# Optimization experiments

Hardware: AMD Instinct MI355X
Metric: run time of the kernel (lower is better)

## Reference

```python
import jax, jax.numpy as jnp
import numpy as np

H = 128          # input hidden dim
HID = 128        # expert hidden width
OUT = 128        # out_channels
NR = 8           # n_routed
NS = 2           # n_shared
RDIM = 16        # router feature dim


def setup_inputs() -> dict:
    key = jax.random.key(0)
    ks = jax.random.split(key, 11)
    s = 0.05
    x = jax.random.normal(ks[0], (2, 32, 32, 32, H), dtype=jnp.float32)
    # router params
    Wr1 = jax.random.normal(ks[1], (H, RDIM), dtype=jnp.float32) * s
    br1 = jnp.zeros((RDIM,), dtype=jnp.float32)
    Wr2 = jax.random.normal(ks[2], (RDIM, NR), dtype=jnp.float32) * s
    br2 = jnp.zeros((NR,), dtype=jnp.float32)
    # routed expert params, stacked on leading expert axis
    We1 = jax.random.normal(ks[3], (NR, H, HID), dtype=jnp.float32) * s
    be1 = jnp.zeros((NR, HID), dtype=jnp.float32)
    We2 = jax.random.normal(ks[4], (NR, HID, OUT), dtype=jnp.float32) * s
    be2 = jnp.zeros((NR, OUT), dtype=jnp.float32)
    # shared expert params
    Ws1 = jax.random.normal(ks[5], (NS, H, HID), dtype=jnp.float32) * s
    bs1 = jnp.zeros((NS, HID), dtype=jnp.float32)
    Ws2 = jax.random.normal(ks[6], (NS, HID, OUT), dtype=jnp.float32) * s
    bs2 = jnp.zeros((NS, OUT), dtype=jnp.float32)
    return dict(x=x, Wr1=Wr1, br1=br1, Wr2=Wr2, br2=br2,
                We1=We1, be1=be1, We2=We2, be2=be2,
                Ws1=Ws1, bs1=bs1, Ws2=Ws2, bs2=bs2)


def reference(x, Wr1, br1, Wr2, br2, We1, be1, We2, be2, Ws1, bs1, Ws2, bs2):
    # router: Dense(16) -> relu -> Dense(n_routed) -> softmax
    rf = jax.nn.relu(jnp.einsum('...h,hr->...r', x, Wr1) + br1)
    logits = jnp.einsum('...r,re->...e', rf, Wr2) + br2
    gate = jax.nn.softmax(logits, axis=-1)                      # [..., NR]
    threshold = 1.0 / NR
    mask = (gate > threshold).astype(gate.dtype)
    mg = gate * mask
    mg = mg / (jnp.sum(mg, axis=-1, keepdims=True) + 1e-8)
    # routed experts (batched over expert axis e): Dense -> gelu(tanh) -> Dense
    hr = jax.nn.gelu(jnp.einsum('...h,ehd->...ed', x, We1) + be1)   # [..., NR, HID]
    ro = jnp.einsum('...ed,edo->...eo', hr, We2) + be2              # [..., NR, OUT]
    routed_agg = jnp.einsum('...eo,...e->...o', ro, mg)
    # shared experts summed
    hs = jax.nn.gelu(jnp.einsum('...h,ehd->...ed', x, Ws1) + bs1)   # [..., NS, HID]
    so = jnp.einsum('...ed,edo->...eo', hs, Ws2) + bs2              # [..., NS, OUT]
    shared_agg = jnp.sum(so, axis=-2)
    return routed_agg + shared_agg
```

## Files before the change

### kernel.cpp

```cpp
#include <hip/hip_runtime.h>
#include <hip/hip_bf16.h>

typedef __bf16 bf16x8 __attribute__((ext_vector_type(8)));
typedef __bf16 bf16x4 __attribute__((ext_vector_type(4)));
typedef float  f32x16 __attribute__((ext_vector_type(16)));
typedef float  f32x4  __attribute__((ext_vector_type(4)));
typedef float  f32x2  __attribute__((ext_vector_type(2)));

static __device__ __forceinline__ f32x16 mfma32(bf16x8 a, bf16x8 b, f32x16 c) {
    return __builtin_amdgcn_mfma_f32_32x32x16_bf16(a, b, c, 0, 0, 0);
}

#define GELU_C1 2.30220820f
#define GELU_C2 0.10294324f

__global__ __launch_bounds__(256) void pack_kernel(
    const float* __restrict__ We1, const float* __restrict__ be1,
    const float* __restrict__ Ws1, const float* __restrict__ bs1,
    const float* __restrict__ We2, const float* __restrict__ Ws2,
    const float* __restrict__ Wr1, const float* __restrict__ br1,
    const float* __restrict__ Wr2, const float* __restrict__ br2,
    __bf16* __restrict__ w1p, __bf16* __restrict__ w2p,
    double* __restrict__ wr1d, double* __restrict__ br1d,
    double* __restrict__ wr2d, double* __restrict__ br2d)
{
    int tid = blockIdx.x * 256 + threadIdx.x;
    if (tid < 23040) {
        int l  = tid & 63;
        int ks = (tid >> 6) % 9;
        int nt = (tid / 576) & 3;
        int e  = tid / 2304;
        const float* src = (e < 8) ? (We1 + e * 16384) : (Ws1 + (e - 8) * 16384);
        const float* bia = (e < 8) ? (be1 + e * 128)   : (bs1 + (e - 8) * 128);
        int n = nt * 32 + (l & 31);
        int kb = ks * 16 + (l >> 5) * 8;
        bf16x8 v;
        #pragma unroll
        for (int j = 0; j < 8; ++j) {
            int k = kb + j;
            float f = (k < 128) ? src[k * 128 + n] : ((k == 128) ? bia[n] : 0.f);
            v[j] = (__bf16)f;
        }
        *(bf16x8*)(w1p + (size_t)tid * 8) = v;
    } else if (tid < 43520) {
        int t2 = tid - 23040;
        int l  = t2 & 63;
        int ks = (t2 >> 6) & 7;
        int ot = (t2 / 512) & 3;
        int e  = t2 / 2048;
        const float* src = (e < 8) ? (We2 + e * 16384) : (Ws2 + (e - 8) * 16384);
        int o  = ot * 32 + (l & 31);
        int lh = l >> 5;
        bf16x8 v;
        #pragma unroll
        for (int j = 0; j < 8; ++j) {
            int hid = 16 * ks + 8 * (j >> 2) + 4 * lh + (j & 3);
            v[j] = (__bf16)src[hid * 128 + o];
        }
        *(bf16x8*)(w2p + (size_t)t2 * 8) = v;
    } else if (tid < 45568) {
        int i = tid - 43520;
        wr1d[i] = (double)Wr1[i];
    } else if (tid < 45696) {
        int i = tid - 45568;
        wr2d[i] = (double)Wr2[i];
    } else if (tid < 45712) {
        int i = tid - 45696;
        br1d[i] = (double)br1[i];
    } else if (tid < 45720) {
        int i = tid - 45712;
        br2d[i] = (double)br2[i];
    }
}

__global__ __launch_bounds__(256) void router_kernel(
    const float* __restrict__ x,
    const double* __restrict__ wr1d, const double* __restrict__ br1d,
    const double* __restrict__ wr2d, const double* __restrict__ br2d,
    float* __restrict__ gates)
{
    __shared__ __align__(16) char lds[41472];
    float*  xs  = (float*)lds;
    double* rfs = (double*)(lds + 33280);

    const int t    = threadIdx.x;
    const int tok0 = blockIdx.x * 64;

    #pragma unroll
    for (int i = 0; i < 8; ++i) {
        int cid = i * 256 + t;
        int m = cid >> 5;
        int c = cid & 31;
        f32x4 v = *(const f32x4*)(x + (size_t)(tok0 + m) * 128 + c * 4);
        f32x2 s0, s1;
        s0[0] = v[0]; s0[1] = v[1]; s1[0] = v[2]; s1[1] = v[3];
        *(f32x2*)(xs + m * 130 + c * 4)     = s0;
        *(f32x2*)(xs + m * 130 + c * 4 + 2) = s1;
    }
    __syncthreads();

    {
        const int tok = t & 63;
        const int rq  = (t >> 6) * 4;
        const int rqs = __builtin_amdgcn_readfirstlane(rq);
        double rf4[4];
        #pragma unroll
        for (int j = 0; j < 4; ++j) rf4[j] = br1d[rqs + j];
        const float* xr = xs + tok * 130;
        #pragma unroll 4
        for (int c = 0; c < 64; ++c) {
            f32x2 xv2 = *(const f32x2*)(xr + c * 2);
            #pragma unroll
            for (int q = 0; q < 2; ++q) {
                double xv = (double)xv2[q];
                int k = c * 2 + q;
                #pragma unroll
                for (int j = 0; j < 4; ++j)
                    rf4[j] = fma(xv, wr1d[k * 16 + rqs + j], rf4[j]);
            }
        }
        #pragma unroll
        for (int j = 0; j < 4; ++j)
            rfs[tok * 16 + rq + j] = rf4[j] > 0.0 ? rf4[j] : 0.0;
    }
    __syncthreads();

    if (t < 64) {
        double lg[8];
        #pragma unroll
        for (int j = 0; j < 8; ++j) lg[j] = br2d[j];
        #pragma unroll
        for (int r = 0; r < 16; ++r) {
            double rv = rfs[t * 16 + r];
            #pragma unroll
            for (int j = 0; j < 8; ++j)
                lg[j] = fma(rv, wr2d[r * 8 + j], lg[j]);
        }
        double mx = lg[0];
        #pragma unroll
        for (int j = 1; j < 8; ++j) mx = lg[j] > mx ? lg[j] : mx;
        double ex[8]; double s = 0.0;
        #pragma unroll
        for (int j = 0; j < 8; ++j) { ex[j] = exp(lg[j] - mx); s += ex[j]; }
        double ms = 0.0;
        bool mk[8];
        #pragma unroll
        for (int j = 0; j < 8; ++j) {
            mk[j] = (8.0 * ex[j] > s);
            ms += mk[j] ? ex[j] : 0.0;
        }
        double inv = 1.0 / (ms + s * 1e-8);
        f32x4 o0, o1;
        #pragma unroll
        for (int j = 0; j < 4; ++j) {
            o0[j] = mk[j]     ? (float)(ex[j] * inv)     : 0.f;
            o1[j] = mk[4 + j] ? (float)(ex[4 + j] * inv) : 0.f;
        }
        *(f32x4*)(gates + (size_t)(tok0 + t) * 8)     = o0;
        *(f32x4*)(gates + (size_t)(tok0 + t) * 8 + 4) = o1;
    }
}

__global__ __launch_bounds__(256, 4) void moe_main_kernel(
    const float* __restrict__ x, const float* __restrict__ gates,
    const __bf16* __restrict__ w1p, const __bf16* __restrict__ w2p,
    const float* __restrict__ be2, const float* __restrict__ bs2,
    float* __restrict__ out)
{
    __shared__ __align__(16) char lds[34816];
    __bf16* Xp = (__bf16*)lds;
    __bf16* Hs = (__bf16*)(lds + 18432);

    const int t    = threadIdx.x;
    const int lane = t & 63;
    const int wave = t >> 6;
    const int l31  = lane & 31;
    const int hi   = lane >> 5;
    const int mt   = wave >> 1;
    const int oh   = wave & 1;
    const int tok0 = blockIdx.x * 64;

    #pragma unroll
    for (int i = 0; i < 4; ++i) {
        int g = i * 256 + t;
        int m = g >> 4;
        int c = g & 15;
        const f32x4* sp = (const f32x4*)(x + (size_t)(tok0 + m) * 128 + c * 8);
        f32x4 va = sp[0], vb = sp[1];
        bf16x8 v;
        v[0]=(__bf16)va[0]; v[1]=(__bf16)va[1]; v[2]=(__bf16)va[2]; v[3]=(__bf16)va[3];
        v[4]=(__bf16)vb[0]; v[5]=(__bf16)vb[1]; v[6]=(__bf16)vb[2]; v[7]=(__bf16)vb[3];
        *(bf16x8*)&Xp[(((m >> 5) * 9 + (c >> 1)) * 64 + (c & 1) * 32 + (m & 31)) * 8] = v;
    }
    if (t < 128) {
        int mtx = t >> 6, l = t & 63;
        bf16x8 v;
        #pragma unroll
        for (int j = 0; j < 8; ++j) v[j] = (__bf16)0.f;
        if (l < 32) v[0] = (__bf16)1.0f;
        *(bf16x8*)&Xp[((mtx * 9 + 8) * 64 + l) * 8] = v;
    }
    __syncthreads();

    const float* gtp = gates + (size_t)(tok0 + 32 * mt + l31) * 8;
    f32x4 ga4 = *(const f32x4*)gtp;
    f32x4 gb4 = *(const f32x4*)(gtp + 4);
    float gte[8] = {ga4[0], ga4[1], ga4[2], ga4[3], gb4[0], gb4[1], gb4[2], gb4[3]};

    f32x16 acc0, acc1;
    #pragma unroll
    for (int i = 0; i < 16; ++i) { acc0[i] = 0.f; acc1[i] = 0.f; }

    const bf16x8* w1v = (const bf16x8*)w1p;
    const bf16x8* w2v = (const bf16x8*)w2p;

    #pragma unroll 1
    for (int e = 0; e < 10; ++e) {
        const float gv = (e < 8) ? gte[e] : 1.0f;

        #pragma unroll
        for (int nti = 0; nti < 2; ++nti) {
            const int nt = 2 * oh + nti;
            const bf16x8* wp = w1v + ((size_t)(e * 4 + nt) * 9) * 64 + lane;
            bf16x8 wb[9];
            #pragma unroll
            for (int ks = 0; ks < 9; ++ks) wb[ks] = wp[ks * 64];
            f32x16 a1;
            #pragma unroll
            for (int i = 0; i < 16; ++i) a1[i] = 0.f;
            #pragma unroll
            for (int ks = 0; ks < 9; ++ks) {
                bf16x8 xb = *(const bf16x8*)&Xp[((mt * 9 + ks) * 64 + lane) * 8];
                a1 = mfma32(wb[ks], xb, a1);
            }
            #pragma unroll
            for (int g4 = 0; g4 < 4; ++g4) {
                bf16x4 pk;
                #pragma unroll
                for (int qp = 0; qp < 2; ++qp) {
                    float h0 = a1[4 * g4 + 2 * qp];
                    float h1 = a1[4 * g4 + 2 * qp + 1];
                    float t0 = h0 * h0, t1 = h1 * h1;
                    float p0 = fmaf(t0, -GELU_C2, -GELU_C1);
                    float p1 = fmaf(t1, -GELU_C2, -GELU_C1);
                    float m0 = h0 * p0, m1 = h1 * p1;
                    float e0 = __builtin_amdgcn_exp2f(m0);
                    float e1 = __builtin_amdgcn_exp2f(m1);
                    float q0 = __builtin_amdgcn_rcpf(1.f + e0);
                    float q1 = __builtin_amdgcn_rcpf(1.f + e1);
                    pk[2 * qp]     = (__bf16)(h0 * q0 * gv);
                    pk[2 * qp + 1] = (__bf16)(h1 * q1 * gv);
                }
                *(bf16x4*)&Hs[((mt * 8 + 2 * nt + (g4 >> 1)) * 64 + lane) * 8
                              + 4 * (g4 & 1)] = pk;
            }
        }
        __syncthreads();

        {
            const bf16x8* wBp = w2v + ((size_t)e * 32 + (2 * oh) * 8) * 64 + lane;
            #pragma unroll
            for (int kq = 0; kq < 8; ++kq) {
                bf16x8 hf = *(const bf16x8*)&Hs[((mt * 8 + kq) * 64 + lane) * 8];
                bf16x8 wB0 = wBp[kq * 64];
                bf16x8 wB1 = wBp[(8 + kq) * 64];
                acc0 = mfma32(hf, wB0, acc0);
                acc1 = mfma32(hf, wB1, acc1);
            }
        }
        __syncthreads();
    }

    {
        float be2c[2][8], bsc[2];
        #pragma unroll
        for (int oti = 0; oti < 2; ++oti) {
            int o = 32 * (2 * oh + oti) + l31;
            bsc[oti] = bs2[o] + bs2[128 + o];
            #pragma unroll
            for (int ee = 0; ee < 8; ++ee) be2c[oti][ee] = be2[ee * 128 + o];
        }
        const float* mgb = gates + (size_t)(tok0 + 32 * mt) * 8;
        #pragma unroll
        for (int r = 0; r < 16; ++r) {
            int mrow = (r & 3) + 8 * (r >> 2) + 4 * hi;
            f32x4 g0 = *(const f32x4*)&mgb[mrow * 8];
            f32x4 g1 = *(const f32x4*)&mgb[mrow * 8 + 4];
            size_t orow = (size_t)(tok0 + 32 * mt + mrow) * 128;
            float b0 = bsc[0], b1 = bsc[1];
            #pragma unroll
            for (int ee = 0; ee < 4; ++ee) {
                b0 = fmaf(g0[ee], be2c[0][ee], b0);
                b1 = fmaf(g0[ee], be2c[1][ee], b1);
            }
            #pragma unroll
            for (int ee = 0; ee < 4; ++ee) {
                b0 = fmaf(g1[ee], be2c[0][4 + ee], b0);
                b1 = fmaf(g1[ee], be2c[1][4 + ee], b1);
            }
            out[orow + 32 * (2 * oh)     + l31] = acc0[r] + b0;
            out[orow + 32 * (2 * oh + 1) + l31] = acc1[r] + b1;
        }
    }
}

extern "C" void kernel_launch(void* const* d_in, const int* in_sizes, int n_in,
                              void* d_out, int out_size, void* d_ws, size_t ws_size,
                              hipStream_t stream)
{
    const float* x   = (const float*)d_in[0];
    const float* Wr1 = (const float*)d_in[1];
    const float* br1 = (const float*)d_in[2];
    const float* Wr2 = (const float*)d_in[3];
    const float* br2 = (const float*)d_in[4];
    const float* We1 = (const float*)d_in[5];
    const float* be1 = (const float*)d_in[6];
    const float* We2 = (const float*)d_in[7];
    const float* be2 = (const float*)d_in[8];
    const float* Ws1 = (const float*)d_in[9];
    const float* bs1 = (const float*)d_in[10];
    const float* Ws2 = (const float*)d_in[11];
    const float* bs2 = (const float*)d_in[12];

    __bf16* w1p  = (__bf16*)d_ws;
    __bf16* w2p  = (__bf16*)((char*)d_ws + 368640);
    double* wr1d = (double*)((char*)d_ws + 696320);
    double* wr2d = (double*)((char*)d_ws + 712704);
    double* br1d = (double*)((char*)d_ws + 713728);
    double* br2d = (double*)((char*)d_ws + 713856);
    float*  gts  = (float*)((char*)d_ws + 720896);

    pack_kernel<<<179, 256, 0, stream>>>(We1, be1, Ws1, bs1, We2, Ws2,
                                         Wr1, br1, Wr2, br2,
                                         w1p, w2p, wr1d, br1d, wr2d, br2d);
    router_kernel<<<1024, 256, 0, stream>>>(x, wr1d, br1d, wr2d, br2d, gts);
    moe_main_kernel<<<1024, 256, 0, stream>>>(x, gts, w1p, w2p, be2, bs2,
                                              (float*)d_out);
}
```

Before: 184.8 us.

## Double token tile per block in MoE kernel and parallelize router softmax

The main MoE kernel now handles 128 tokens per block instead of 64. Each wave keeps its W1 and W2 expert fragments in registers and reuses them across two 32-token M-tiles, which halves global weight traffic per token. The bias row now comes from a register constant instead of an extra K-step stored in LDS, gates are staged in LDS, and the second GEMM runs under raised wave priority. The router spreads the logit and exp work over all 256 threads using padded LDS arrays instead of 64 threads. In exchange the main kernel uses more LDS and registers, occupancy hint drops from 4 to 2 blocks per CU, and the grid halves to 512 blocks.

```diff
diff --git a/kernel.cpp b/kernel.cpp
--- a/kernel.cpp
+++ b/kernel.cpp
@@ -13,6 +13,26 @@
 
 #define GELU_C1 2.30220820f
 #define GELU_C2 0.10294324f
+
+static __device__ __forceinline__ bf16x8 gelu8(f32x16 a, int base, float gv) {
+    bf16x8 r;
+    #pragma unroll
+    for (int p = 0; p < 4; ++p) {
+        f32x2 hh; hh[0] = a[base + 2 * p]; hh[1] = a[base + 2 * p + 1];
+        f32x2 tt = hh * hh;
+        f32x2 pp;
+        pp[0] = fmaf(tt[0], -GELU_C2, -GELU_C1);
+        pp[1] = fmaf(tt[1], -GELU_C2, -GELU_C1);
+        f32x2 mm = hh * pp;
+        float e0 = __builtin_amdgcn_exp2f(mm[0]);
+        float e1 = __builtin_amdgcn_exp2f(mm[1]);
+        float q0 = __builtin_amdgcn_rcpf(1.f + e0);
+        float q1 = __builtin_amdgcn_rcpf(1.f + e1);
+        r[2 * p]     = (__bf16)(hh[0] * q0 * gv);
+        r[2 * p + 1] = (__bf16)(hh[1] * q1 * gv);
+    }
+    return r;
+}
 
 __global__ __launch_bounds__(256) void pack_kernel(
     const float* __restrict__ We1, const float* __restrict__ be1,
@@ -79,9 +99,11 @@
     const double* __restrict__ wr2d, const double* __restrict__ br2d,
     float* __restrict__ gates)
 {
-    __shared__ __align__(16) char lds[41472];
+    __shared__ __align__(16) char lds[51200];
     float*  xs  = (float*)lds;
     double* rfs = (double*)(lds + 33280);
+    double* lgs = (double*)(lds + 41984);
+    double* exs = (double*)(lds + 46592);
 
     const int t    = threadIdx.x;
     const int tok0 = blockIdx.x * 64;
@@ -121,27 +143,39 @@
         }
         #pragma unroll
         for (int j = 0; j < 4; ++j)
-            rfs[tok * 16 + rq + j] = rf4[j] > 0.0 ? rf4[j] : 0.0;
+            rfs[tok * 17 + rqs + j] = rf4[j] > 0.0 ? rf4[j] : 0.0;
+    }
+    __syncthreads();
+
+    const int tok = t & 63;
+    const int j0  = __builtin_amdgcn_readfirstlane((t >> 6) * 2);
+    double lgA = br2d[j0], lgB = br2d[j0 + 1];
+    #pragma unroll
+    for (int r = 0; r < 16; ++r) {
+        double rv = rfs[tok * 17 + r];
+        lgA = fma(rv, wr2d[r * 8 + j0],     lgA);
+        lgB = fma(rv, wr2d[r * 8 + j0 + 1], lgB);
+    }
+    lgs[tok * 9 + j0]     = lgA;
+    lgs[tok * 9 + j0 + 1] = lgB;
+    __syncthreads();
+
+    {
+        double mx = lgs[tok * 9];
+        #pragma unroll
+        for (int k = 1; k < 8; ++k) {
+            double v = lgs[tok * 9 + k];
+            mx = v > mx ? v : mx;
+        }
+        exs[tok * 9 + j0]     = exp(lgA - mx);
+        exs[tok * 9 + j0 + 1] = exp(lgB - mx);
     }
     __syncthreads();
 
     if (t < 64) {
-        double lg[8];
-        #pragma unroll
-        for (int j = 0; j < 8; ++j) lg[j] = br2d[j];
-        #pragma unroll
-        for (int r = 0; r < 16; ++r) {
-            double rv = rfs[t * 16 + r];
-            #pragma unroll
-            for (int j = 0; j < 8; ++j)
-                lg[j] = fma(rv, wr2d[r * 8 + j], lg[j]);
-        }
-        double mx = lg[0];
-        #pragma unroll
-        for (int j = 1; j < 8; ++j) mx = lg[j] > mx ? lg[j] : mx;
         double ex[8]; double s = 0.0;
         #pragma unroll
-        for (int j = 0; j < 8; ++j) { ex[j] = exp(lg[j] - mx); s += ex[j]; }
+        for (int j = 0; j < 8; ++j) { ex[j] = exs[t * 9 + j]; s += ex[j]; }
         double ms = 0.0;
         bool mk[8];
         #pragma unroll
@@ -161,27 +195,28 @@
     }
 }
 
-__global__ __launch_bounds__(256, 4) void moe_main_kernel(
+__global__ __launch_bounds__(256, 2) void moe_main_kernel(
     const float* __restrict__ x, const float* __restrict__ gates,
     const __bf16* __restrict__ w1p, const __bf16* __restrict__ w2p,
     const float* __restrict__ be2, const float* __restrict__ bs2,
     float* __restrict__ out)
 {
-    __shared__ __align__(16) char lds[34816];
+    __shared__ __align__(16) char lds[69632];
     __bf16* Xp = (__bf16*)lds;
-    __bf16* Hs = (__bf16*)(lds + 18432);
+    __bf16* Hs = (__bf16*)(lds + 32768);
+    float*  mg = (float*)(lds + 65536);
 
     const int t    = threadIdx.x;
     const int lane = t & 63;
     const int wave = t >> 6;
     const int l31  = lane & 31;
     const int hi   = lane >> 5;
-    const int mt   = wave >> 1;
+    const int mp   = wave >> 1;
     const int oh   = wave & 1;
-    const int tok0 = blockIdx.x * 64;
-
-    #pragma unroll
-    for (int i = 0; i < 4; ++i) {
+    const int tok0 = blockIdx.x * 128;
+
+    #pragma unroll
+    for (int i = 0; i < 8; ++i) {
         int g = i * 256 + t;
         int m = g >> 4;
         int c = g & 15;
@@ -190,84 +225,79 @@
         bf16x8 v;
         v[0]=(__bf16)va[0]; v[1]=(__bf16)va[1]; v[2]=(__bf16)va[2]; v[3]=(__bf16)va[3];
         v[4]=(__bf16)vb[0]; v[5]=(__bf16)vb[1]; v[6]=(__bf16)vb[2]; v[7]=(__bf16)vb[3];
-        *(bf16x8*)&Xp[(((m >> 5) * 9 + (c >> 1)) * 64 + (c & 1) * 32 + (m & 31)) * 8] = v;
-    }
-    if (t < 128) {
-        int mtx = t >> 6, l = t & 63;
-        bf16x8 v;
-        #pragma unroll
-        for (int j = 0; j < 8; ++j) v[j] = (__bf16)0.f;
-        if (l < 32) v[0] = (__bf16)1.0f;
-        *(bf16x8*)&Xp[((mtx * 9 + 8) * 64 + l) * 8] = v;
-    }
-    __syncthreads();
-
-    const float* gtp = gates + (size_t)(tok0 + 32 * mt + l31) * 8;
-    f32x4 ga4 = *(const f32x4*)gtp;
-    f32x4 gb4 = *(const f32x4*)(gtp + 4);
-    float gte[8] = {ga4[0], ga4[1], ga4[2], ga4[3], gb4[0], gb4[1], gb4[2], gb4[3]};
-
-    f32x16 acc0, acc1;
-    #pragma unroll
-    for (int i = 0; i < 16; ++i) { acc0[i] = 0.f; acc1[i] = 0.f; }
+        *(bf16x8*)&Xp[(((m >> 5) * 8 + (c >> 1)) * 64 + (c & 1) * 32 + (m & 31)) * 8] = v;
+    }
+    {
+        int m = t >> 1, half = t & 1;
+        f32x4 g = *(const f32x4*)(gates + (size_t)(tok0 + m) * 8 + half * 4);
+        *(f32x4*)&mg[m * 8 + half * 4] = g;
+    }
+    __syncthreads();
+
+    bf16x8 xbias;
+    #pragma unroll
+    for (int j = 0; j < 8; ++j) xbias[j] = (__bf16)0.f;
+    if (lane < 32) xbias[0] = (__bf16)1.0f;
+
+    f32x16 acc00, acc01, acc10, acc11;
+    #pragma unroll
+    for (int i = 0; i < 16; ++i) { acc00[i]=0.f; acc01[i]=0.f; acc10[i]=0.f; acc11[i]=0.f; }
 
     const bf16x8* w1v = (const bf16x8*)w1p;
     const bf16x8* w2v = (const bf16x8*)w2p;
 
     #pragma unroll 1
     for (int e = 0; e < 10; ++e) {
-        const float gv = (e < 8) ? gte[e] : 1.0f;
-
-        #pragma unroll
-        for (int nti = 0; nti < 2; ++nti) {
-            const int nt = 2 * oh + nti;
-            const bf16x8* wp = w1v + ((size_t)(e * 4 + nt) * 9) * 64 + lane;
-            bf16x8 wb[9];
-            #pragma unroll
-            for (int ks = 0; ks < 9; ++ks) wb[ks] = wp[ks * 64];
-            f32x16 a1;
-            #pragma unroll
-            for (int i = 0; i < 16; ++i) a1[i] = 0.f;
-            #pragma unroll
-            for (int ks = 0; ks < 9; ++ks) {
-                bf16x8 xb = *(const bf16x8*)&Xp[((mt * 9 + ks) * 64 + lane) * 8];
-                a1 = mfma32(wb[ks], xb, a1);
+        const bf16x8* wp  = w1v + ((size_t)(e * 4 + 2 * oh) * 9) * 64 + lane;
+        const bf16x8* wBp = w2v + ((size_t)(e * 4 + 2 * oh) * 8) * 64 + lane;
+        bf16x8 wb0[9], wb1[9];
+        #pragma unroll
+        for (int ks = 0; ks < 9; ++ks) wb0[ks] = wp[ks * 64];
+        #pragma unroll
+        for (int ks = 0; ks < 9; ++ks) wb1[ks] = wp[(9 + ks) * 64];
+        bf16x8 wB0[8];
+        #pragma unroll
+        for (int kq = 0; kq < 8; ++kq) wB0[kq] = wBp[kq * 64];
+
+        #pragma unroll
+        for (int mi = 0; mi < 2; ++mi) {
+            const int mt = 2 * mp + mi;
+            float gv = 1.0f;
+            if (e < 8) gv = mg[(32 * mt + l31) * 8 + e];
+            f32x16 a0, a1;
+            #pragma unroll
+            for (int i = 0; i < 16; ++i) { a0[i] = 0.f; a1[i] = 0.f; }
+            #pragma unroll
+            for (int ks = 0; ks < 8; ++ks) {
+                bf16x8 xb = *(const bf16x8*)&Xp[((mt * 8 + ks) * 64 + lane) * 8];
+                a0 = mfma32(wb0[ks], xb, a0);
+                a1 = mfma32(wb1[ks], xb, a1);
             }
-            #pragma unroll
-            for (int g4 = 0; g4 < 4; ++g4) {
-                bf16x4 pk;
-                #pragma unroll
-                for (int qp = 0; qp < 2; ++qp) {
-                    float h0 = a1[4 * g4 + 2 * qp];
-                    float h1 = a1[4 * g4 + 2 * qp + 1];
-                    float t0 = h0 * h0, t1 = h1 * h1;
-                    float p0 = fmaf(t0, -GELU_C2, -GELU_C1);
-                    float p1 = fmaf(t1, -GELU_C2, -GELU_C1);
-                    float m0 = h0 * p0, m1 = h1 * p1;
-                    float e0 = __builtin_amdgcn_exp2f(m0);
-                    float e1 = __builtin_amdgcn_exp2f(m1);
-                    float q0 = __builtin_amdgcn_rcpf(1.f + e0);
-                    float q1 = __builtin_amdgcn_rcpf(1.f + e1);
-                    pk[2 * qp]     = (__bf16)(h0 * q0 * gv);
-                    pk[2 * qp + 1] = (__bf16)(h1 * q1 * gv);
-                }
-                *(bf16x4*)&Hs[((mt * 8 + 2 * nt + (g4 >> 1)) * 64 + lane) * 8
-                              + 4 * (g4 & 1)] = pk;
-            }
+            a0 = mfma32(wb0[8], xbias, a0);
+            a1 = mfma32(wb1[8], xbias, a1);
+            int rb = (mt * 8 + 4 * oh) * 64 + lane;
+            *(bf16x8*)&Hs[(rb + 0 * 64) * 8] = gelu8(a0, 0, gv);
+            *(bf16x8*)&Hs[(rb + 1 * 64) * 8] = gelu8(a0, 8, gv);
+            *(bf16x8*)&Hs[(rb + 2 * 64) * 8] = gelu8(a1, 0, gv);
+            *(bf16x8*)&Hs[(rb + 3 * 64) * 8] = gelu8(a1, 8, gv);
         }
         __syncthreads();
 
-        {
-            const bf16x8* wBp = w2v + ((size_t)e * 32 + (2 * oh) * 8) * 64 + lane;
-            #pragma unroll
-            for (int kq = 0; kq < 8; ++kq) {
-                bf16x8 hf = *(const bf16x8*)&Hs[((mt * 8 + kq) * 64 + lane) * 8];
-                bf16x8 wB0 = wBp[kq * 64];
-                bf16x8 wB1 = wBp[(8 + kq) * 64];
-                acc0 = mfma32(hf, wB0, acc0);
-                acc1 = mfma32(hf, wB1, acc1);
-            }
-        }
+        bf16x8 wB1[8];
+        #pragma unroll
+        for (int kq = 0; kq < 8; ++kq) wB1[kq] = wBp[(8 + kq) * 64];
+
+        __builtin_amdgcn_s_setprio(1);
+        #pragma unroll
+        for (int kq = 0; kq < 8; ++kq) {
+            bf16x8 h0 = *(const bf16x8*)&Hs[(((2 * mp)     * 8 + kq) * 64 + lane) * 8];
+            bf16x8 h1 = *(const bf16x8*)&Hs[(((2 * mp + 1) * 8 + kq) * 64 + lane) * 8];
+            acc00 = mfma32(h0, wB0[kq], acc00);
+            acc01 = mfma32(h0, wB1[kq], acc01);
+            acc10 = mfma32(h1, wB0[kq], acc10);
+            acc11 = mfma32(h1, wB1[kq], acc11);
+        }
+        __builtin_amdgcn_s_setprio(0);
         __syncthreads();
     }
 
@@ -280,26 +310,32 @@
             #pragma unroll
             for (int ee = 0; ee < 8; ++ee) be2c[oti][ee] = be2[ee * 128 + o];
         }
-        const float* mgb = gates + (size_t)(tok0 + 32 * mt) * 8;
-        #pragma unroll
-        for (int r = 0; r < 16; ++r) {
-            int mrow = (r & 3) + 8 * (r >> 2) + 4 * hi;
-            f32x4 g0 = *(const f32x4*)&mgb[mrow * 8];
-            f32x4 g1 = *(const f32x4*)&mgb[mrow * 8 + 4];
-            size_t orow = (size_t)(tok0 + 32 * mt + mrow) * 128;
-            float b0 = bsc[0], b1 = bsc[1];
-            #pragma unroll
-            for (int ee = 0; ee < 4; ++ee) {
-                b0 = fmaf(g0[ee], be2c[0][ee], b0);
-                b1 = fmaf(g0[ee], be2c[1][ee], b1);
+        #pragma unroll
+        for (int mi = 0; mi < 2; ++mi) {
+            const int mt = 2 * mp + mi;
+            const float* mgb = mg + (32 * mt) * 8;
+            f32x16 aA = mi ? acc10 : acc00;
+            f32x16 aB = mi ? acc11 : acc01;
+            #pragma unroll
+            for (int r = 0; r < 16; ++r) {
+                int mrow = (r & 3) + 8 * (r >> 2) + 4 * hi;
+                f32x4 g0 = *(const f32x4*)&mgb[mrow * 8];
+                f32x4 g1 = *(const f32x4*)&mgb[mrow * 8 + 4];
+                size_t orow = (size_t)(tok0 + 32 * mt + mrow) * 128;
+                float b0 = bsc[0], b1 = bsc[1];
+                #pragma unroll
+                for (int ee = 0; ee < 4; ++ee) {
+                    b0 = fmaf(g0[ee], be2c[0][ee], b0);
+                    b1 = fmaf(g0[ee], be2c[1][ee], b1);
+                }
+                #pragma unroll
+                for (int ee = 0; ee < 4; ++ee) {
+                    b0 = fmaf(g1[ee], be2c[0][4 + ee], b0);
+                    b1 = fmaf(g1[ee], be2c[1][4 + ee], b1);
+                }
+                out[orow + 32 * (2 * oh)     + l31] = aA[r] + b0;
+                out[orow + 32 * (2 * oh + 1) + l31] = aB[r] + b1;
             }
-            #pragma unroll
-            for (int ee = 0; ee < 4; ++ee) {
-                b0 = fmaf(g1[ee], be2c[0][4 + ee], b0);
-                b1 = fmaf(g1[ee], be2c[1][4 + ee], b1);
-            }
-            out[orow + 32 * (2 * oh)     + l31] = acc0[r] + b0;
-            out[orow + 32 * (2 * oh + 1) + l31] = acc1[r] + b1;
         }
     }
 }
@@ -334,6 +370,6 @@
                                          Wr1, br1, Wr2, br2,
                                          w1p, w2p, wr1d, br1d, wr2d, br2d);
     router_kernel<<<1024, 256, 0, stream>>>(x, wr1d, br1d, wr2d, br2d, gts);
-    moe_main_kernel<<<1024, 256, 0, stream>>>(x, gts, w1p, w2p, be2, bs2,
-                                              (float*)d_out);
-}
+    moe_main_kernel<<<512, 256, 0, stream>>>(x, gts, w1p, w2p, be2, bs2,
+                                             (float*)d_out);
+}
```

Result: no change. 184.5 us (-0.1%).
